# Kernel optimization log

Hardware: AMD Instinct MI355X
Metric: run time of the kernel (lower is better)

The kernel has to match this reference:

```python
import jax, jax.numpy as jnp
import numpy as np

N, E, D, H = 100000, 1250000, 64, 128
EPS = 1e-5


def sage_bn_relu(x, src, dst, W_self, b_self, W_neigh, gamma, beta):
    # mean aggregation over in-neighbors (DGL SAGEConv 'mean')
    n = x.shape[0]
    deg = jax.ops.segment_sum(jnp.ones((src.shape[0],), x.dtype), dst, num_segments=n)
    agg = jax.ops.segment_sum(x[src], dst, num_segments=n)  # [N, d]
    neigh = agg / jnp.maximum(deg, 1.0)[:, None]             # zero in-degree -> 0
    h = x @ W_self + b_self + neigh @ W_neigh                # fc_self + fc_neigh
    # BatchNorm1d (training-mode batch statistics, biased variance)
    mu = h.mean(0)
    var = jnp.mean((h - mu) ** 2, axis=0)
    h = (h - mu) * jax.lax.rsqrt(var + EPS) * gamma + beta
    return jax.nn.relu(h)  # dropout omitted (deterministic eval)


def setup_inputs() -> dict:
    key = jax.random.key(0)
    ks = jax.random.split(key, 32)
    inp = {
        "x": jax.random.normal(ks[0], (N, D), jnp.float32),
        "src": jax.random.randint(ks[1], (E,), 0, N),
        "dst": jax.random.randint(ks[2], (E,), 0, N),
    }
    dims = [(D, H), (H, H), (H, H)]
    k = 3
    for i, (din, dout) in enumerate(dims):
        s = 1.0 / np.sqrt(din)
        inp[f"W_self{i}"] = jax.random.uniform(ks[k], (din, dout), jnp.float32, -s, s); k += 1
        inp[f"b_self{i}"] = jnp.zeros((dout,), jnp.float32)
        inp[f"W_neigh{i}"] = jax.random.uniform(ks[k], (din, dout), jnp.float32, -s, s); k += 1
        inp[f"gamma{i}"] = jnp.ones((dout,), jnp.float32)
        inp[f"beta{i}"] = jnp.zeros((dout,), jnp.float32)
    s = 1.0 / np.sqrt(H)
    inp["Wc"] = jax.random.uniform(ks[k], (H, 2), jnp.float32, -s, s)
    inp["bc"] = jnp.zeros((2,), jnp.float32)
    return inp


def reference(x, src, dst,
              W_self0, b_self0, W_neigh0, gamma0, beta0,
              W_self1, b_self1, W_neigh1, gamma1, beta1,
              W_self2, b_self2, W_neigh2, gamma2, beta2,
              Wc, bc):
    h = sage_bn_relu(x, src, dst, W_self0, b_self0, W_neigh0, gamma0, beta0)
    h = sage_bn_relu(h, src, dst, W_self1, b_self1, W_neigh1, gamma1, beta1)
    h = sage_bn_relu(h, src, dst, W_self2, b_self2, W_neigh2, gamma2, beta2)
    return h @ Wc + bc  # [N, 2]
```

## Files before the change

### kernel.cpp

```cpp
#include <hip/hip_runtime.h>


#define N_NODES 100000
#define N_EDGES 1250000
#define NB 782
#define BSZ 128
#define CAP 2048
#define BPART 256
#define INVN (1.0f / 100000.0f)

typedef short bf16x8 __attribute__((ext_vector_type(8)));
typedef float f32x4 __attribute__((ext_vector_type(4)));
typedef unsigned short u16x8 __attribute__((ext_vector_type(8)));
typedef unsigned short u16x4 __attribute__((ext_vector_type(4)));

__device__ __forceinline__ float bf2f(unsigned short u) {
  union { unsigned int i; float f; } c; c.i = ((unsigned int)u) << 16; return c.f;
}
__device__ __forceinline__ unsigned short f2bf(float f) {
  union { float f; unsigned int i; } c; c.f = f;
  unsigned int r = (c.i + 0x7FFFu + ((c.i >> 16) & 1u)) >> 16;
  return (unsigned short)r;
}
__device__ __forceinline__ void bn_st(const float* stats, const float* gam,
                                      const float* bet, int c, float& s, float& t) {
  float sum = stats[c] + stats[256 + c] + stats[512 + c] + stats[768 + c];
  float sq  = stats[128 + c] + stats[384 + c] + stats[640 + c] + stats[896 + c];
  float mu = sum * INVN;
  float var = sq * INVN - mu * mu;
  s = gam[c] * rsqrtf(var + 1e-5f);
  t = bet[c] - mu * s;
}
__device__ __forceinline__ void gload_lds16(const void* g, void* l) {
  __builtin_amdgcn_global_load_lds(
      (const __attribute__((address_space(1))) unsigned int*)g,
      (__attribute__((address_space(3))) unsigned int*)l, 16, 0, 0);
}
template <int DIN>
__device__ __forceinline__ int nswz(int row, int c) {
  return row * DIN + (c ^ ((row & (DIN == 128 ? 15 : 7)) << 3));
}

__global__ __launch_bounds__(256) void k_prep(
    const float* __restrict__ x, unsigned short* __restrict__ x16,
    const float* __restrict__ W0s, const float* __restrict__ W0n,
    const float* __restrict__ W1s, const float* __restrict__ W1n,
    const float* __restrict__ W2s, const float* __restrict__ W2n,
    unsigned short* __restrict__ wt, float* __restrict__ stats3,
    const int* __restrict__ dst, int* __restrict__ hist, int E) {
  __shared__ int hh[NB];
  int blk = blockIdx.x, t = threadIdx.x;
  if (blk < 6250) {
    int i = blk * 256 + t;
    float4 v = ((const float4*)x)[i];
    u16x4 o;
    o.x = f2bf(v.x); o.y = f2bf(v.y); o.z = f2bf(v.z); o.w = f2bf(v.w);
    ((u16x4*)x16)[i] = o;
  } else if (blk < 6570) {
    int i = (blk - 6250) * 256 + t;
    if (i < 16384) {
      const float* W = (i < 8192) ? W0s : W0n;
      unsigned short* o = wt + (i < 8192 ? 0 : 8192);
      int j = i & 8191;
      int c = j >> 6, k = j & 63;
      o[j] = f2bf(W[k * 128 + c]);
    } else {
      int j = i - 16384;
      int sel = j >> 14;
      j &= 16383;
      const float* W = (sel == 0) ? W1s : (sel == 1) ? W1n : (sel == 2) ? W2s : W2n;
      unsigned short* o = wt + 16384 + sel * 16384;
      int c = j >> 7, k = j & 127;
      o[j] = f2bf(W[k * 128 + c]);
    }
  } else if (blk == 6570) {
    for (int i = t; i < 3 * 1024; i += 256) stats3[i] = 0.f;
  } else {
    int hb = blk - 6571;
    int chunk = (E + BPART - 1) / BPART;
    int start = hb * chunk;
    int end = min(E, start + chunk);
    for (int b = t; b < NB; b += 256) hh[b] = 0;
    __syncthreads();
    for (int e = start + t; e < end; e += 256) atomicAdd(&hh[dst[e] >> 7], 1);
    __syncthreads();
    for (int b = t; b < NB; b += 256) hist[hb * NB + b] = hh[b];
  }
}

__global__ __launch_bounds__(256) void k_scan(const int* __restrict__ hist,
                                              int* __restrict__ base,
                                              int* __restrict__ gcursor) {
  int bb = blockIdx.x * 256 + threadIdx.x;
  if (bb >= NB) return;
  int run = 0;
  for (int r0 = 0; r0 < BPART; r0 += 16) {
    int v[16];
    #pragma unroll
    for (int u = 0; u < 16; u++) v[u] = hist[(r0 + u) * NB + bb];
    #pragma unroll
    for (int u = 0; u < 16; u++) { base[(r0 + u) * NB + bb] = run; run += v[u]; }
  }
  gcursor[bb] = run;
}

__global__ __launch_bounds__(256) void k_scatter(const int* __restrict__ src,
                                                 const int* __restrict__ dst,
                                                 const int* __restrict__ base,
                                                 unsigned int* __restrict__ part, int E) {
  __shared__ int cur[NB];
  int t = threadIdx.x;
  int chunk = (E + BPART - 1) / BPART;
  int start = blockIdx.x * chunk;
  int end = min(E, start + chunk);
  for (int b = t; b < NB; b += 256) cur[b] = base[blockIdx.x * NB + b];
  __syncthreads();
  for (int e = start + t; e < end; e += 256) {
    int d = dst[e];
    int b = d >> 7;
    int pos = atomicAdd(&cur[b], 1);
    if ((unsigned)pos < (unsigned)CAP)
      part[(size_t)b * CAP + pos] = (unsigned)src[e] | ((unsigned)(d & 127) << 17);
  }
}

template <int DIN, bool BN>
__global__ __launch_bounds__(256) void k_layer(
    const unsigned short* __restrict__ h, const unsigned short* __restrict__ W1t,
    const unsigned short* __restrict__ W2t, const float* __restrict__ bias,
    const unsigned int* __restrict__ part, const int* __restrict__ gcursor,
    unsigned short* __restrict__ C, float* __restrict__ stats, int M,
    const float* __restrict__ statsP, const float* __restrict__ gamP,
    const float* __restrict__ betP) {
  __shared__ unsigned short As[2][128 * 32];
  __shared__ unsigned short Bs[2][128 * 32];
  __shared__ unsigned short neighT[128 * DIN];
  __shared__ unsigned eord[CAP];
  __shared__ int cnt[BSZ], offv[BSZ], cur[BSZ];
  __shared__ float sBN[128], tBN[128];
  unsigned* eraw = (unsigned*)&As[0][0];
  float* redS = (float*)&eord[0];
  float* redQ = redS + 512;

  int t = threadIdx.x;
  int lane = t & 63, w = t >> 6;
  int l15 = lane & 15, quad = lane >> 4;
  int bkt = blockIdx.x;
  int node0 = bkt * BSZ;
  int row0 = node0;
  int nn = min(BSZ, M - node0);

  if (t < BSZ) cnt[t] = 0;
  if (BN && t < 128) bn_st(statsP, gamP, betP, t, sBN[t], tBN[t]);
  __syncthreads();
  int ec = gcursor[bkt];
  ec = max(0, min(ec, CAP));
  for (int i = t; i < ec; i += 256) {
    unsigned wd = part[(size_t)bkt * CAP + i];
    eraw[i] = wd;
    atomicAdd(&cnt[wd >> 17], 1);
  }
  __syncthreads();
  if (t < BSZ) offv[t] = cnt[t];
  __syncthreads();
  #pragma unroll
  for (int o = 1; o < BSZ; o <<= 1) {
    int xv = 0;
    if (t < BSZ && t >= o) xv = offv[t - o];
    __syncthreads();
    if (t < BSZ) offv[t] += xv;
    __syncthreads();
  }
  if (t < BSZ) { int ex = offv[t] - cnt[t]; offv[t] = ex; cur[t] = ex; }
  __syncthreads();
  for (int i = t; i < ec; i += 256) {
    unsigned wd = eraw[i];
    int p = atomicAdd(&cur[wd >> 17], 1);
    eord[p] = wd & 0x1FFFF;
  }
  __syncthreads();

  const int G = DIN / 8, NG = 256 / G;
  int gid = t / G, li = t % G;
  float sreg[8], treg[8];
  if (BN) {
    #pragma unroll
    for (int k = 0; k < 8; k++) { sreg[k] = sBN[li * 8 + k]; treg[k] = tBN[li * 8 + k]; }
  }
  for (int nd = gid; nd < BSZ; nd += NG) {
    u16x8 o;
    if (nd >= nn) {
      #pragma unroll
      for (int k = 0; k < 8; k++) o[k] = 0;
    } else {
      int s0 = offv[nd], c = cnt[nd];
      int e = s0 + c;
      float acc[8] = {0.f, 0.f, 0.f, 0.f, 0.f, 0.f, 0.f, 0.f};
      int j = s0;
      for (; j + 4 <= e; j += 4) {
        int a0 = eord[j], a1 = eord[j + 1], a2 = eord[j + 2], a3 = eord[j + 3];
        u16x8 v0 = *(const u16x8*)&h[(size_t)a0 * DIN + li * 8];
        u16x8 v1 = *(const u16x8*)&h[(size_t)a1 * DIN + li * 8];
        u16x8 v2 = *(const u16x8*)&h[(size_t)a2 * DIN + li * 8];
        u16x8 v3 = *(const u16x8*)&h[(size_t)a3 * DIN + li * 8];
        if (BN) {
          #pragma unroll
          for (int k = 0; k < 8; k++)
            acc[k] += fmaxf(fmaf(bf2f(v0[k]), sreg[k], treg[k]), 0.f)
                    + fmaxf(fmaf(bf2f(v1[k]), sreg[k], treg[k]), 0.f)
                    + fmaxf(fmaf(bf2f(v2[k]), sreg[k], treg[k]), 0.f)
                    + fmaxf(fmaf(bf2f(v3[k]), sreg[k], treg[k]), 0.f);
        } else {
          #pragma unroll
          for (int k = 0; k < 8; k++)
            acc[k] += (bf2f(v0[k]) + bf2f(v1[k])) + (bf2f(v2[k]) + bf2f(v3[k]));
        }
      }
      for (; j < e; j++) {
        int a0 = eord[j];
        u16x8 v0 = *(const u16x8*)&h[(size_t)a0 * DIN + li * 8];
        #pragma unroll
        for (int k = 0; k < 8; k++) {
          float f = bf2f(v0[k]);
          acc[k] += BN ? fmaxf(fmaf(f, sreg[k], treg[k]), 0.f) : f;
        }
      }
      float inv = 1.0f / fmaxf((float)c, 1.0f);
      #pragma unroll
      for (int k = 0; k < 8; k++) o[k] = f2bf(acc[k] * inv);
    }
    *(u16x8*)&neighT[nswz<DIN>(nd, li * 8)] = o;
  }
  __syncthreads();

  const int steps1 = DIN / 32;
  const int S = steps1 * 2;
  f32x4 acc[2][8];
  #pragma unroll
  for (int rt = 0; rt < 2; rt++)
    #pragma unroll
    for (int ct = 0; ct < 8; ct++) acc[rt][ct] = (f32x4){0.f, 0.f, 0.f, 0.f};

  auto stageA = [&](int s, int bi) {
    int k0 = s * 32;
    #pragma unroll
    for (int i = 0; i < 2; i++) {
      int idx = t + 256 * i;
      int r = idx >> 2, prt = idx & 3;
      gload_lds16(&h[(size_t)(row0 + r) * DIN + k0 + prt * 8],
                  &As[bi][(i * 256 + w * 64) * 8]);
    }
  };
  auto stageB = [&](int s, int bi) {
    const unsigned short* Wt = (s < steps1) ? W1t : W2t;
    int k0 = (s < steps1 ? s : s - steps1) * 32;
    #pragma unroll
    for (int i = 0; i < 2; i++) {
      int idx = t + 256 * i;
      int r = idx >> 2, prt = idx & 3;
      gload_lds16(&Wt[(size_t)r * DIN + k0 + prt * 8],
                  &Bs[bi][(i * 256 + w * 64) * 8]);
    }
  };
  u16x8 vreg[2];
  auto bnLoad = [&](int s) {
    int k0 = s * 32;
    #pragma unroll
    for (int i = 0; i < 2; i++) {
      int idx = t + 256 * i;
      int r = idx >> 2, prt = idx & 3;
      int row = row0 + r;
      vreg[i] = (u16x8){0, 0, 0, 0, 0, 0, 0, 0};
      if (row < M) vreg[i] = *(const u16x8*)&h[(size_t)row * DIN + k0 + prt * 8];
    }
  };
  auto bnWrite = [&](int s, int bi) {
    int k0 = s * 32;
    #pragma unroll
    for (int i = 0; i < 2; i++) {
      int idx = t + 256 * i;
      int prt = idx & 3;
      u16x8 v = vreg[i];
      #pragma unroll
      for (int j2 = 0; j2 < 8; j2++) {
        int c = k0 + prt * 8 + j2;
        v[j2] = f2bf(fmaxf(fmaf(bf2f(v[j2]), sBN[c], tBN[c]), 0.f));
      }
      *(u16x8*)&As[bi][idx * 8] = v;
    }
  };

  if (BN) { bnLoad(0); stageB(0, 0); bnWrite(0, 0); }
  else    { stageA(0, 0); stageB(0, 0); }
  __syncthreads();

  int cb = 0;
  for (int s = 0; s < S; s++) {
    int nb = cb ^ 1;
    bool haveNext = (s + 1 < S);
    bool nextA1 = (s + 1 < steps1);
    if (haveNext) {
      if (nextA1) { if (BN) bnLoad(s + 1); else stageA(s + 1, nb); }
      stageB(s + 1, nb);
    }
    bf16x8 af[2], bfr[8];
    if (s < steps1) {
      #pragma unroll
      for (int rt = 0; rt < 2; rt++)
        af[rt] = *(const bf16x8*)&As[cb][(w * 32 + rt * 16 + l15) * 32 + quad * 8];
    } else {
      int c0 = (s - steps1) * 32 + quad * 8;
      #pragma unroll
      for (int rt = 0; rt < 2; rt++) {
        int row = w * 32 + rt * 16 + l15;
        af[rt] = *(const bf16x8*)&neighT[nswz<DIN>(row, c0)];
      }
    }
    #pragma unroll
    for (int ct = 0; ct < 8; ct++)
      bfr[ct] = *(const bf16x8*)&Bs[cb][(ct * 16 + l15) * 32 + quad * 8];
    #pragma unroll
    for (int rt = 0; rt < 2; rt++)
      #pragma unroll
      for (int ct = 0; ct < 8; ct++)
        acc[rt][ct] = __builtin_amdgcn_mfma_f32_16x16x32_bf16(af[rt], bfr[ct], acc[rt][ct], 0, 0, 0);
    if (haveNext) {
      if (nextA1 && BN) bnWrite(s + 1, nb);
      __syncthreads();
    }
    cb = nb;
  }

  float bcol[8], ls[8], lq[8];
  #pragma unroll
  for (int ct = 0; ct < 8; ct++) {
    bcol[ct] = bias[ct * 16 + l15];
    ls[ct] = 0.f; lq[ct] = 0.f;
  }
  #pragma unroll
  for (int rt = 0; rt < 2; rt++) {
    #pragma unroll
    for (int r = 0; r < 4; r++) {
      int row = row0 + w * 32 + rt * 16 + quad * 4 + r;
      if (row < M) {
        #pragma unroll
        for (int ct = 0; ct < 8; ct++) {
          float v = acc[rt][ct][r] + bcol[ct];
          C[(size_t)row * 128 + ct * 16 + l15] = f2bf(v);
          ls[ct] += v; lq[ct] += v * v;
        }
      }
    }
  }
  #pragma unroll
  for (int ct = 0; ct < 8; ct++) {
    ls[ct] += __shfl_xor(ls[ct], 16); ls[ct] += __shfl_xor(ls[ct], 32);
    lq[ct] += __shfl_xor(lq[ct], 16); lq[ct] += __shfl_xor(lq[ct], 32);
  }
  if (quad == 0) {
    #pragma unroll
    for (int ct = 0; ct < 8; ct++) {
      redS[w * 128 + ct * 16 + l15] = ls[ct];
      redQ[w * 128 + ct * 16 + l15] = lq[ct];
    }
  }
  __syncthreads();
  if (t < 128) {
    float s = redS[t] + redS[128 + t] + redS[256 + t] + redS[384 + t];
    float q = redQ[t] + redQ[128 + t] + redQ[256 + t] + redQ[384 + t];
    int rep = (blockIdx.x & 3) * 256;
    atomicAdd(&stats[rep + t], s);
    atomicAdd(&stats[rep + 128 + t], q);
  }
}

__global__ void k_final(const unsigned short* __restrict__ h,
                        const float* __restrict__ statsP, const float* __restrict__ gamP,
                        const float* __restrict__ betP, const float* __restrict__ Wc,
                        const float* __restrict__ bc, float* __restrict__ out, int n) {
  int lane = threadIdx.x & 63;
  int row = blockIdx.x * (blockDim.x >> 6) + (threadIdx.x >> 6);
  if (row >= n) return;
  float acc0 = 0.f, acc1 = 0.f;
  #pragma unroll
  for (int m = 0; m < 2; m++) {
    int c = lane + 64 * m;
    float s, tt;
    bn_st(statsP, gamP, betP, c, s, tt);
    float v = bf2f(h[(size_t)row * 128 + c]);
    v = fmaxf(fmaf(v, s, tt), 0.f);
    acc0 += v * Wc[c * 2 + 0];
    acc1 += v * Wc[c * 2 + 1];
  }
  #pragma unroll
  for (int off = 32; off > 0; off >>= 1) {
    acc0 += __shfl_down(acc0, off);
    acc1 += __shfl_down(acc1, off);
  }
  if (lane == 0) {
    out[row * 2 + 0] = acc0 + bc[0];
    out[row * 2 + 1] = acc1 + bc[1];
  }
}

extern "C" void kernel_launch(void* const* d_in, const int* in_sizes, int n_in,
                              void* d_out, int out_size, void* d_ws, size_t ws_size,
                              hipStream_t stream) {
  const float* x   = (const float*)d_in[0];
  const int* src   = (const int*)d_in[1];
  const int* dst   = (const int*)d_in[2];
  const float* Wself[3] = {(const float*)d_in[3], (const float*)d_in[8],  (const float*)d_in[13]};
  const float* bself[3] = {(const float*)d_in[4], (const float*)d_in[9],  (const float*)d_in[14]};
  const float* Wngh[3]  = {(const float*)d_in[5], (const float*)d_in[10], (const float*)d_in[15]};
  const float* gam[3]   = {(const float*)d_in[6], (const float*)d_in[11], (const float*)d_in[16]};
  const float* bet[3]   = {(const float*)d_in[7], (const float*)d_in[12], (const float*)d_in[17]};
  const float* Wc = (const float*)d_in[18];
  const float* bc = (const float*)d_in[19];
  float* out = (float*)d_out;

  const int N = N_NODES, E = N_EDGES;

  unsigned short* x16 = (unsigned short*)d_ws;
  unsigned short* b1  = x16 + (size_t)N * 64;
  unsigned short* b2  = b1 + (size_t)N * 128;
  unsigned short* wt  = b2 + (size_t)N * 128;
  unsigned int* part  = (unsigned int*)(wt + 81920);
  int* gcursor  = (int*)(part + (size_t)NB * CAP);
  float* stats3 = (float*)(gcursor + NB);

  int* hist = (int*)b1;
  int* base = hist + (size_t)BPART * NB;

  k_prep<<<6571 + BPART, 256, 0, stream>>>(x, x16, Wself[0], Wngh[0], Wself[1],
                                           Wngh[1], Wself[2], Wngh[2], wt, stats3,
                                           dst, hist, E);

  k_scan<<<(NB + 255) / 256, 256, 0, stream>>>(hist, base, gcursor);
  k_scatter<<<BPART, 256, 0, stream>>>(src, dst, base, part, E);

  k_layer<64, false><<<NB, 256, 0, stream>>>(
      x16, wt + 0, wt + 8192, bself[0], part, gcursor, b1, stats3 + 0, N,
      nullptr, nullptr, nullptr);
  k_layer<128, true><<<NB, 256, 0, stream>>>(
      b1, wt + 16384, wt + 32768, bself[1], part, gcursor, b2, stats3 + 1024, N,
      stats3 + 0, gam[0], bet[0]);
  k_layer<128, true><<<NB, 256, 0, stream>>>(
      b2, wt + 49152, wt + 65536, bself[2], part, gcursor, b1, stats3 + 2048, N,
      stats3 + 1024, gam[1], bet[1]);

  k_final<<<(N + 3) / 4, 256, 0, stream>>>(b1, stats3 + 2048, gam[2], bet[2],
                                           Wc, bc, out, N);
}
```

Baseline: 411.6 us.

## Halve node buckets, use 512-thread blocks with work-stealing aggregation and split-column MFMA

Node buckets shrink from 128 to 64 (NB 1563, CAP 1024), and each layer block now runs 512 threads. Each thread group takes neighbor rows dynamically through an LDS work-stealing counter, and the gather loop unrolls by 2 instead of 4. The GEMM drops the double-buffered A/B staging. A fragments now load straight from global or from neighT, and each wave computes one 16-row strip by 64-column half using a single-buffered B tile. The goal is less LDS use, higher occupancy and better load balance, at the cost of losing the prefetch overlap in the GEMM.

```diff
diff --git a/kernel.cpp b/kernel.cpp
--- a/kernel.cpp
+++ b/kernel.cpp
@@ -3,9 +3,9 @@
 
 #define N_NODES 100000
 #define N_EDGES 1250000
-#define NB 782
-#define BSZ 128
-#define CAP 2048
+#define NB 1563
+#define BSZ 64
+#define CAP 1024
 #define BPART 256
 #define INVN (1.0f / 100000.0f)
 
@@ -35,10 +35,6 @@
   __builtin_amdgcn_global_load_lds(
       (const __attribute__((address_space(1))) unsigned int*)g,
       (__attribute__((address_space(3))) unsigned int*)l, 16, 0, 0);
-}
-template <int DIN>
-__device__ __forceinline__ int nswz(int row, int c) {
-  return row * DIN + (c ^ ((row & (DIN == 128 ? 15 : 7)) << 3));
 }
 
 __global__ __launch_bounds__(256) void k_prep(
@@ -82,7 +78,7 @@
     int end = min(E, start + chunk);
     for (int b = t; b < NB; b += 256) hh[b] = 0;
     __syncthreads();
-    for (int e = start + t; e < end; e += 256) atomicAdd(&hh[dst[e] >> 7], 1);
+    for (int e = start + t; e < end; e += 256) atomicAdd(&hh[dst[e] >> 6], 1);
     __syncthreads();
     for (int b = t; b < NB; b += 256) hist[hb * NB + b] = hh[b];
   }
@@ -117,45 +113,47 @@
   __syncthreads();
   for (int e = start + t; e < end; e += 256) {
     int d = dst[e];
-    int b = d >> 7;
+    int b = d >> 6;
     int pos = atomicAdd(&cur[b], 1);
     if ((unsigned)pos < (unsigned)CAP)
-      part[(size_t)b * CAP + pos] = (unsigned)src[e] | ((unsigned)(d & 127) << 17);
+      part[(size_t)b * CAP + pos] = (unsigned)src[e] | ((unsigned)(d & 63) << 17);
   }
 }
 
 template <int DIN, bool BN>
-__global__ __launch_bounds__(256) void k_layer(
+__global__ __launch_bounds__(512, 8) void k_layer(
     const unsigned short* __restrict__ h, const unsigned short* __restrict__ W1t,
     const unsigned short* __restrict__ W2t, const float* __restrict__ bias,
     const unsigned int* __restrict__ part, const int* __restrict__ gcursor,
     unsigned short* __restrict__ C, float* __restrict__ stats, int M,
     const float* __restrict__ statsP, const float* __restrict__ gamP,
     const float* __restrict__ betP) {
-  __shared__ unsigned short As[2][128 * 32];
-  __shared__ unsigned short Bs[2][128 * 32];
-  __shared__ unsigned short neighT[128 * DIN];
+  __shared__ unsigned short neighT[64 * DIN];
   __shared__ unsigned eord[CAP];
+  __shared__ unsigned short Bs[128 * 32];
   __shared__ int cnt[BSZ], offv[BSZ], cur[BSZ];
+  __shared__ int stealCtr;
   __shared__ float sBN[128], tBN[128];
-  unsigned* eraw = (unsigned*)&As[0][0];
-  float* redS = (float*)&eord[0];
+  unsigned* eraw = (unsigned*)neighT;
+  float* redS = (float*)eord;
   float* redQ = redS + 512;
 
+  constexpr int SWZM = (DIN == 128) ? 15 : 7;
   int t = threadIdx.x;
   int lane = t & 63, w = t >> 6;
   int l15 = lane & 15, quad = lane >> 4;
   int bkt = blockIdx.x;
   int node0 = bkt * BSZ;
-  int row0 = node0;
   int nn = min(BSZ, M - node0);
 
   if (t < BSZ) cnt[t] = 0;
+  if (t == 0) stealCtr = 0;
   if (BN && t < 128) bn_st(statsP, gamP, betP, t, sBN[t], tBN[t]);
   __syncthreads();
+
   int ec = gcursor[bkt];
   ec = max(0, min(ec, CAP));
-  for (int i = t; i < ec; i += 256) {
+  for (int i = t; i < ec; i += 512) {
     unsigned wd = part[(size_t)bkt * CAP + i];
     eraw[i] = wd;
     atomicAdd(&cnt[wd >> 17], 1);
@@ -173,202 +171,151 @@
   }
   if (t < BSZ) { int ex = offv[t] - cnt[t]; offv[t] = ex; cur[t] = ex; }
   __syncthreads();
-  for (int i = t; i < ec; i += 256) {
+  for (int i = t; i < ec; i += 512) {
     unsigned wd = eraw[i];
     int p = atomicAdd(&cur[wd >> 17], 1);
     eord[p] = wd & 0x1FFFF;
   }
   __syncthreads();
 
-  const int G = DIN / 8, NG = 256 / G;
-  int gid = t / G, li = t % G;
+  const int G = DIN / 8;
+  int li = t & (G - 1);
   float sreg[8], treg[8];
   if (BN) {
     #pragma unroll
     for (int k = 0; k < 8; k++) { sreg[k] = sBN[li * 8 + k]; treg[k] = tBN[li * 8 + k]; }
   }
-  for (int nd = gid; nd < BSZ; nd += NG) {
+  for (;;) {
+    int nd0 = 0;
+    if (li == 0) nd0 = atomicAdd(&stealCtr, 1);
+    int nd = __shfl(nd0, 0, G);
+    if (nd >= BSZ) break;
     u16x8 o;
     if (nd >= nn) {
       #pragma unroll
       for (int k = 0; k < 8; k++) o[k] = 0;
     } else {
-      int s0 = offv[nd], c = cnt[nd];
-      int e = s0 + c;
+      int s = offv[nd], c = cnt[nd];
+      int e = s + c;
       float acc[8] = {0.f, 0.f, 0.f, 0.f, 0.f, 0.f, 0.f, 0.f};
-      int j = s0;
-      for (; j + 4 <= e; j += 4) {
-        int a0 = eord[j], a1 = eord[j + 1], a2 = eord[j + 2], a3 = eord[j + 3];
-        u16x8 v0 = *(const u16x8*)&h[(size_t)a0 * DIN + li * 8];
-        u16x8 v1 = *(const u16x8*)&h[(size_t)a1 * DIN + li * 8];
-        u16x8 v2 = *(const u16x8*)&h[(size_t)a2 * DIN + li * 8];
-        u16x8 v3 = *(const u16x8*)&h[(size_t)a3 * DIN + li * 8];
+      int j = s;
+      for (; j + 2 <= e; j += 2) {
+        int sn0 = eord[j], sn1 = eord[j + 1];
+        u16x8 v0 = *(const u16x8*)&h[(size_t)sn0 * DIN + li * 8];
+        u16x8 v1 = *(const u16x8*)&h[(size_t)sn1 * DIN + li * 8];
         if (BN) {
           #pragma unroll
           for (int k = 0; k < 8; k++)
             acc[k] += fmaxf(fmaf(bf2f(v0[k]), sreg[k], treg[k]), 0.f)
-                    + fmaxf(fmaf(bf2f(v1[k]), sreg[k], treg[k]), 0.f)
-                    + fmaxf(fmaf(bf2f(v2[k]), sreg[k], treg[k]), 0.f)
-                    + fmaxf(fmaf(bf2f(v3[k]), sreg[k], treg[k]), 0.f);
+                    + fmaxf(fmaf(bf2f(v1[k]), sreg[k], treg[k]), 0.f);
         } else {
           #pragma unroll
+          for (int k = 0; k < 8; k++) acc[k] += bf2f(v0[k]) + bf2f(v1[k]);
+        }
+      }
+      if (j < e) {
+        int sn = eord[j];
+        u16x8 v = *(const u16x8*)&h[(size_t)sn * DIN + li * 8];
+        if (BN) {
+          #pragma unroll
           for (int k = 0; k < 8; k++)
-            acc[k] += (bf2f(v0[k]) + bf2f(v1[k])) + (bf2f(v2[k]) + bf2f(v3[k]));
-        }
-      }
-      for (; j < e; j++) {
-        int a0 = eord[j];
-        u16x8 v0 = *(const u16x8*)&h[(size_t)a0 * DIN + li * 8];
-        #pragma unroll
-        for (int k = 0; k < 8; k++) {
-          float f = bf2f(v0[k]);
-          acc[k] += BN ? fmaxf(fmaf(f, sreg[k], treg[k]), 0.f) : f;
+            acc[k] += fmaxf(fmaf(bf2f(v[k]), sreg[k], treg[k]), 0.f);
+        } else {
+          #pragma unroll
+          for (int k = 0; k < 8; k++) acc[k] += bf2f(v[k]);
         }
       }
       float inv = 1.0f / fmaxf((float)c, 1.0f);
       #pragma unroll
       for (int k = 0; k < 8; k++) o[k] = f2bf(acc[k] * inv);
     }
-    *(u16x8*)&neighT[nswz<DIN>(nd, li * 8)] = o;
-  }
-  __syncthreads();
-
-  const int steps1 = DIN / 32;
-  const int S = steps1 * 2;
-  f32x4 acc[2][8];
-  #pragma unroll
-  for (int rt = 0; rt < 2; rt++)
-    #pragma unroll
-    for (int ct = 0; ct < 8; ct++) acc[rt][ct] = (f32x4){0.f, 0.f, 0.f, 0.f};
-
-  auto stageA = [&](int s, int bi) {
-    int k0 = s * 32;
-    #pragma unroll
-    for (int i = 0; i < 2; i++) {
-      int idx = t + 256 * i;
-      int r = idx >> 2, prt = idx & 3;
-      gload_lds16(&h[(size_t)(row0 + r) * DIN + k0 + prt * 8],
-                  &As[bi][(i * 256 + w * 64) * 8]);
-    }
-  };
-  auto stageB = [&](int s, int bi) {
-    const unsigned short* Wt = (s < steps1) ? W1t : W2t;
-    int k0 = (s < steps1 ? s : s - steps1) * 32;
-    #pragma unroll
-    for (int i = 0; i < 2; i++) {
-      int idx = t + 256 * i;
-      int r = idx >> 2, prt = idx & 3;
-      gload_lds16(&Wt[(size_t)r * DIN + k0 + prt * 8],
-                  &Bs[bi][(i * 256 + w * 64) * 8]);
-    }
-  };
-  u16x8 vreg[2];
-  auto bnLoad = [&](int s) {
-    int k0 = s * 32;
-    #pragma unroll
-    for (int i = 0; i < 2; i++) {
-      int idx = t + 256 * i;
-      int r = idx >> 2, prt = idx & 3;
-      int row = row0 + r;
-      vreg[i] = (u16x8){0, 0, 0, 0, 0, 0, 0, 0};
-      if (row < M) vreg[i] = *(const u16x8*)&h[(size_t)row * DIN + k0 + prt * 8];
-    }
-  };
-  auto bnWrite = [&](int s, int bi) {
-    int k0 = s * 32;
-    #pragma unroll
-    for (int i = 0; i < 2; i++) {
-      int idx = t + 256 * i;
-      int prt = idx & 3;
-      u16x8 v = vreg[i];
+    *(u16x8*)&neighT[nd * DIN + ((li * 8) ^ ((nd & SWZM) << 3))] = o;
+  }
+  __syncthreads();
+
+  const int strip = w >> 1;
+  const int ch = w & 1;
+  const int row = strip * 16 + l15;
+  f32x4 acc4[4];
+  #pragma unroll
+  for (int ct = 0; ct < 4; ct++) acc4[ct] = (f32x4){0.f, 0.f, 0.f, 0.f};
+
+  #pragma unroll
+  for (int half = 0; half < 2; half++) {
+    const unsigned short* Wt = half ? W2t : W1t;
+    for (int k0 = 0; k0 < DIN; k0 += 32) {
+      {
+        int r = t >> 2, prt = t & 3;
+        gload_lds16(&Wt[(size_t)r * DIN + k0 + prt * 8], &Bs[(w * 64) * 8]);
+      }
+      __syncthreads();
+      bf16x8 af;
+      {
+        u16x8 v;
+        if (half == 0) {
+          v = *(const u16x8*)&h[(size_t)(node0 + row) * DIN + k0 + quad * 8];
+          if (BN) {
+            #pragma unroll
+            for (int j = 0; j < 8; j++) {
+              int c = k0 + quad * 8 + j;
+              v[j] = f2bf(fmaxf(fmaf(bf2f(v[j]), sBN[c], tBN[c]), 0.f));
+            }
+          }
+        } else {
+          int cc = k0 + quad * 8;
+          v = *(const u16x8*)&neighT[row * DIN + (cc ^ ((row & SWZM) << 3))];
+        }
+        af = *(bf16x8*)&v;
+      }
       #pragma unroll
-      for (int j2 = 0; j2 < 8; j2++) {
-        int c = k0 + prt * 8 + j2;
-        v[j2] = f2bf(fmaxf(fmaf(bf2f(v[j2]), sBN[c], tBN[c]), 0.f));
-      }
-      *(u16x8*)&As[bi][idx * 8] = v;
-    }
-  };
-
-  if (BN) { bnLoad(0); stageB(0, 0); bnWrite(0, 0); }
-  else    { stageA(0, 0); stageB(0, 0); }
-  __syncthreads();
-
-  int cb = 0;
-  for (int s = 0; s < S; s++) {
-    int nb = cb ^ 1;
-    bool haveNext = (s + 1 < S);
-    bool nextA1 = (s + 1 < steps1);
-    if (haveNext) {
-      if (nextA1) { if (BN) bnLoad(s + 1); else stageA(s + 1, nb); }
-      stageB(s + 1, nb);
-    }
-    bf16x8 af[2], bfr[8];
-    if (s < steps1) {
+      for (int ct = 0; ct < 4; ct++) {
+        bf16x8 bfr = *(const bf16x8*)&Bs[(ch * 64 + ct * 16 + l15) * 32 + quad * 8];
+        acc4[ct] = __builtin_amdgcn_mfma_f32_16x16x32_bf16(af, bfr, acc4[ct], 0, 0, 0);
+      }
+      __syncthreads();
+    }
+  }
+
+  float bcol[4], ls[4], lq[4];
+  #pragma unroll
+  for (int ct = 0; ct < 4; ct++) {
+    bcol[ct] = bias[ch * 64 + ct * 16 + l15];
+    ls[ct] = 0.f; lq[ct] = 0.f;
+  }
+  #pragma unroll
+  for (int r = 0; r < 4; r++) {
+    int orow = node0 + strip * 16 + quad * 4 + r;
+    if (orow < M) {
       #pragma unroll
-      for (int rt = 0; rt < 2; rt++)
-        af[rt] = *(const bf16x8*)&As[cb][(w * 32 + rt * 16 + l15) * 32 + quad * 8];
-    } else {
-      int c0 = (s - steps1) * 32 + quad * 8;
-      #pragma unroll
-      for (int rt = 0; rt < 2; rt++) {
-        int row = w * 32 + rt * 16 + l15;
-        af[rt] = *(const bf16x8*)&neighT[nswz<DIN>(row, c0)];
-      }
-    }
-    #pragma unroll
-    for (int ct = 0; ct < 8; ct++)
-      bfr[ct] = *(const bf16x8*)&Bs[cb][(ct * 16 + l15) * 32 + quad * 8];
-    #pragma unroll
-    for (int rt = 0; rt < 2; rt++)
-      #pragma unroll
-      for (int ct = 0; ct < 8; ct++)
-        acc[rt][ct] = __builtin_amdgcn_mfma_f32_16x16x32_bf16(af[rt], bfr[ct], acc[rt][ct], 0, 0, 0);
-    if (haveNext) {
-      if (nextA1 && BN) bnWrite(s + 1, nb);
-      __syncthreads();
-    }
-    cb = nb;
-  }
-
-  float bcol[8], ls[8], lq[8];
-  #pragma unroll
-  for (int ct = 0; ct < 8; ct++) {
-    bcol[ct] = bias[ct * 16 + l15];
-    ls[ct] = 0.f; lq[ct] = 0.f;
-  }
-  #pragma unroll
-  for (int rt = 0; rt < 2; rt++) {
-    #pragma unroll
-    for (int r = 0; r < 4; r++) {
-      int row = row0 + w * 32 + rt * 16 + quad * 4 + r;
-      if (row < M) {
-        #pragma unroll
-        for (int ct = 0; ct < 8; ct++) {
-          float v = acc[rt][ct][r] + bcol[ct];
-          C[(size_t)row * 128 + ct * 16 + l15] = f2bf(v);
-          ls[ct] += v; lq[ct] += v * v;
-        }
-      }
-    }
-  }
-  #pragma unroll
-  for (int ct = 0; ct < 8; ct++) {
+      for (int ct = 0; ct < 4; ct++) {
+        float v = acc4[ct][r] + bcol[ct];
+        C[(size_t)orow * 128 + ch * 64 + ct * 16 + l15] = f2bf(v);
+        ls[ct] += v; lq[ct] += v * v;
+      }
+    }
+  }
+  #pragma unroll
+  for (int ct = 0; ct < 4; ct++) {
     ls[ct] += __shfl_xor(ls[ct], 16); ls[ct] += __shfl_xor(ls[ct], 32);
     lq[ct] += __shfl_xor(lq[ct], 16); lq[ct] += __shfl_xor(lq[ct], 32);
   }
   if (quad == 0) {
     #pragma unroll
-    for (int ct = 0; ct < 8; ct++) {
-      redS[w * 128 + ct * 16 + l15] = ls[ct];
-      redQ[w * 128 + ct * 16 + l15] = lq[ct];
+    for (int ct = 0; ct < 4; ct++) {
+      redS[w * 64 + ct * 16 + l15] = ls[ct];
+      redQ[w * 64 + ct * 16 + l15] = lq[ct];
     }
   }
   __syncthreads();
   if (t < 128) {
-    float s = redS[t] + redS[128 + t] + redS[256 + t] + redS[384 + t];
-    float q = redQ[t] + redQ[128 + t] + redQ[256 + t] + redQ[384 + t];
-    int rep = (blockIdx.x & 3) * 256;
+    int ch2 = t >> 6, c6 = t & 63;
+    float s = 0.f, q = 0.f;
+    #pragma unroll
+    for (int st = 0; st < 4; st++) {
+      s += redS[(st * 2 + ch2) * 64 + c6];
+      q += redQ[(st * 2 + ch2) * 64 + c6];
+    }
+    int rep = (bkt & 3) * 256;
     atomicAdd(&stats[rep + t], s);
     atomicAdd(&stats[rep + 128 + t], q);
   }
@@ -421,7 +368,8 @@
   const int N = N_NODES, E = N_EDGES;
 
   unsigned short* x16 = (unsigned short*)d_ws;
-  unsigned short* b1  = x16 + (size_t)N * 64;
+  unsigned short* b0  = x16 + (size_t)N * 64;
+  unsigned short* b1  = b0 + (size_t)N * 128;
   unsigned short* b2  = b1 + (size_t)N * 128;
   unsigned short* wt  = b2 + (size_t)N * 128;
   unsigned int* part  = (unsigned int*)(wt + 81920);
@@ -431,20 +379,20 @@
   int* hist = (int*)b1;
   int* base = hist + (size_t)BPART * NB;
 
-  k_prep<<<6571 + BPART, 256, 0, stream>>>(x, x16, Wself[0], Wngh[0], Wself[1],
-                                           Wngh[1], Wself[2], Wngh[2], wt, stats3,
-                                           dst, hist, E);
+  k_prep<<<6571 + BPART, 256, 0, stream>>>(
+      x, x16, Wself[0], Wngh[0], Wself[1], Wngh[1], Wself[2], Wngh[2],
+      wt, stats3, dst, hist, E);
 
   k_scan<<<(NB + 255) / 256, 256, 0, stream>>>(hist, base, gcursor);
   k_scatter<<<BPART, 256, 0, stream>>>(src, dst, base, part, E);
 
-  k_layer<64, false><<<NB, 256, 0, stream>>>(
+  k_layer<64, false><<<NB, 512, 0, stream>>>(
       x16, wt + 0, wt + 8192, bself[0], part, gcursor, b1, stats3 + 0, N,
       nullptr, nullptr, nullptr);
-  k_layer<128, true><<<NB, 256, 0, stream>>>(
+  k_layer<128, true><<<NB, 512, 0, stream>>>(
       b1, wt + 16384, wt + 32768, bself[1], part, gcursor, b2, stats3 + 1024, N,
       stats3 + 0, gam[0], bet[0]);
-  k_layer<128, true><<<NB, 256, 0, stream>>>(
+  k_layer<128, true><<<NB, 512, 0, stream>>>(
       b2, wt + 49152, wt + 65536, bself[2], part, gcursor, b1, stats3 + 2048, N,
       stats3 + 1024, gam[1], bet[1]);
 
```

After: 375.9 us. -8.7%, faster.
